# Performance work log

Hardware: AMD Instinct MI355X
Metric: run time of the kernel (lower is better)

## Reference

```python
import jax, jax.numpy as jnp
import numpy as np

_N = 512
_L = 65536


def setup_inputs() -> dict:
    key = jax.random.key(0)
    ks = jax.random.split(key, 11)
    N, L = _N, _L
    sc = 1.0 / np.sqrt(N)  # lecun-normal style scaling
    f = lambda k, s: jax.random.normal(k, s, dtype=jnp.float32)
    return {
        # stable DPLR spectrum: negative real parts
        "Lambda_re": -(jax.random.uniform(ks[0], (N,), dtype=jnp.float32) + 0.1),
        "Lambda_im": f(ks[1], (N,)),
        "p_re": f(ks[2], (N,)), "p_im": f(ks[3], (N,)),
        "q_re": f(ks[4], (N,)), "q_im": f(ks[5], (N,)),
        "Vc_re": f(ks[6], (N, N)) * sc, "Vc_im": f(ks[7], (N, N)) * sc,
        "Ct": f(ks[8], (1, N, 2)) * sc,
        "B": f(ks[9], (N, 1)) * sc,
        "log_step": jax.random.uniform(ks[10], (1,), dtype=jnp.float32)
                    * (np.log(0.1) - np.log(0.001)) + np.log(0.001),
        "L": L,
    }


def reference(Lambda_re, Lambda_im, p_re, p_im, q_re, q_im,
              Vc_re, Vc_im, Ct, B, log_step, L):
    Lambda = Lambda_re + 1j * Lambda_im            # (N,)
    p = p_re + 1j * p_im                           # (N,)
    q = q_re + 1j * q_im                           # (N,)
    Vc = Vc_re + 1j * Vc_im                        # (N,N)
    Ct_c = Ct[..., 0] + 1j * Ct[..., 1]            # (1,N)
    Bc = (Vc @ B.astype(Vc.dtype)).ravel()         # (N,) complex, B = Vc @ B
    step = jnp.exp(log_step)[0]

    # aterm = (Ct*, q*), bterm = (B, p)
    a0 = Ct_c.conj().ravel()
    a1 = q.conj()
    b0 = Bc
    b1 = p

    # roots of unity
    Omega = jnp.exp(-2j * jnp.pi * (jnp.arange(L) / L))   # (L,)
    g = (2.0 / step) * ((1.0 - Omega) / (1.0 + Omega))    # (L,) bilinear transform
    c = 2.0 / (1.0 + Omega)                               # (L,)

    # single fused Cauchy pass: resolvent (L,N) contracted with all 4 rank-1 terms
    r = 1.0 / (g[:, None] - Lambda[None, :])               # (L,N)
    terms = jnp.stack([a0 * b0, a0 * b1, a1 * b0, a1 * b1], axis=1)  # (N,4)
    K = r @ terms                                          # (L,4): k00,k01,k10,k11
    k00, k01, k10, k11 = K[:, 0], K[:, 1], K[:, 2], K[:, 3]

    atRoots = c * (k00 - k01 * (1.0 / (1.0 + k11)) * k10)  # Woodbury correction
    out = jnp.fft.ifft(atRoots, L).reshape(L)
    return out.real
```

## Files before the change

### kernel.cpp

```cpp
#include <hip/hip_runtime.h>
#include <math.h>

constexpr int WS_TERMS = 0;
constexpr int WS_ZT    = 8192;

__device__ __forceinline__ float sin2pi(float x) { return __builtin_amdgcn_sinf(x); }
__device__ __forceinline__ float cos2pi(float x) { return __builtin_amdgcn_cosf(x); }

__global__ __launch_bounds__(256) void k_setup(
    const float* __restrict__ Lr, const float* __restrict__ Li,
    const float* __restrict__ pr, const float* __restrict__ pi,
    const float* __restrict__ qr, const float* __restrict__ qi,
    const float* __restrict__ Vr, const float* __restrict__ Vi,
    const float* __restrict__ Ct, const float* __restrict__ Bv,
    const float* __restrict__ log_step,
    float* __restrict__ terms)
{
    __shared__ float red[8];
    int n = blockIdx.x;
    int t = threadIdx.x;
    float b0 = Bv[t], b1 = Bv[t + 256];
    float sr = fmaf(Vr[n*512 + t], b0, Vr[n*512 + t + 256] * b1);
    float si = fmaf(Vi[n*512 + t], b0, Vi[n*512 + t + 256] * b1);
    #pragma unroll
    for (int off = 32; off > 0; off >>= 1) {
        sr += __shfl_down(sr, off, 64);
        si += __shfl_down(si, off, 64);
    }
    if ((t & 63) == 0) { red[(t >> 6)*2] = sr; red[(t >> 6)*2 + 1] = si; }
    __syncthreads();
    if (t == 0) {
        float b0r = red[0] + red[2] + red[4] + red[6];
        float b0i = red[1] + red[3] + red[5] + red[7];
        double step = exp((double)log_step[0]);
        float t2s = (float)(2.0 / step);
        float lr  = Lr[n];
        float a0r = Ct[2*n], a0i = -Ct[2*n+1];
        float a1r = qr[n],   a1i = -qi[n];
        float b1r = pr[n],   b1i = pi[n];
        float* tm = terms + n * 12;
        tm[0]  = -lr;                 tm[1]  = Li[n];
        tm[2]  = a0r*b0r - a0i*b0i;   tm[3]  = a0r*b0i + a0i*b0r;
        tm[4]  = a0r*b1r - a0i*b1i;   tm[5]  = a0r*b1i + a0i*b1r;
        tm[6]  = a1r*b0r - a1i*b0i;   tm[7]  = a1r*b0i + a1i*b0r;
        tm[8]  = a1r*b1r - a1i*b1i;   tm[9]  = a1r*b1i + a1i*b1r;
        tm[10] = lr*lr;               tm[11] = t2s;
    }
}

__global__ __launch_bounds__(512, 8) void k_mainA(
    const float* __restrict__ terms,
    float* __restrict__ ZTf)
{
    __shared__ float buf[6144];
    int tid = threadIdx.x;
    int b   = blockIdx.x;
    int l1      = b >> 2;
    int quarter = b & 3;

    {
        float4* dst = (float4*)buf;
        const float4* src = (const float4*)terms;
        #pragma unroll
        for (int i = 0; i < 3; ++i) dst[tid + 512*i] = src[tid + 512*i];
    }

    int u     = tid & 63;
    int chunk = tid >> 6;
    int l2    = quarter*64 + u;
    int l     = l1 + 256*l2;

    float tv2 = (float)l * (1.0f / 131072.0f);
    float sn  = sin2pi(tv2), cn = cos2pi(tv2);
    float T   = sn / cn;
    __syncthreads();
    float t2s = buf[11];
    float g_i = t2s * T;
    if (!(fabsf(T) <= 1.0e6f)) { g_i = 3e30f; T = 0.f; }

    float ac[8];
    #pragma unroll
    for (int c = 0; c < 8; ++c) ac[c] = 0.f;

    const float4* t4 = (const float4*)buf + chunk * 64 * 3;
    #pragma unroll 4
    for (int n = 0; n < 64; ++n) {
        float4 Aq = t4[n*3 + 0];
        float4 Bq = t4[n*3 + 1];
        float4 Cq = t4[n*3 + 2];
        float di = g_i - Aq.y;
        float dd = fmaf(di, di, Cq.z);
        float iv = __builtin_amdgcn_rcpf(dd);
        float rr = Aq.x * iv;
        float ri = -di * iv;
        ac[0] = fmaf(rr, Aq.z, ac[0]); ac[0] = fmaf(-ri, Aq.w, ac[0]);
        ac[1] = fmaf(rr, Aq.w, ac[1]); ac[1] = fmaf( ri, Aq.z, ac[1]);
        ac[2] = fmaf(rr, Bq.x, ac[2]); ac[2] = fmaf(-ri, Bq.y, ac[2]);
        ac[3] = fmaf(rr, Bq.y, ac[3]); ac[3] = fmaf( ri, Bq.x, ac[3]);
        ac[4] = fmaf(rr, Bq.z, ac[4]); ac[4] = fmaf(-ri, Bq.w, ac[4]);
        ac[5] = fmaf(rr, Bq.w, ac[5]); ac[5] = fmaf( ri, Bq.z, ac[5]);
        ac[6] = fmaf(rr, Cq.x, ac[6]); ac[6] = fmaf(-ri, Cq.y, ac[6]);
        ac[7] = fmaf(rr, Cq.y, ac[7]); ac[7] = fmaf( ri, Cq.x, ac[7]);
    }
    __syncthreads();

    if (chunk >= 4) {
        float* p = buf + (chunk - 4) * 576 + u * 9;
        #pragma unroll
        for (int c = 0; c < 8; ++c) p[c] = ac[c];
    }
    __syncthreads();
    if (chunk < 4) {
        float* p = buf + chunk * 576 + u * 9;
        #pragma unroll
        for (int c = 0; c < 8; ++c) p[c] += ac[c];
    }
    __syncthreads();

    {
        int a = (tid >> 3) * 9 + (tid & 7);
        buf[2304 + a] = buf[a] + buf[576 + a] + buf[1152 + a] + buf[1728 + a];
    }
    __syncthreads();

    if (tid < 64) {
        const float* rd = buf + 2304 + tid * 9;
        float s0r = rd[0], s0i = rd[1], s1r = rd[2], s1i = rd[3];
        float s2r = rd[4], s2i = rd[5], s3r = rd[6], s3i = rd[7];
        float e1r = 1.f + s3r, e1i = s3i;
        float eiv = 1.0f / fmaf(e1r, e1r, e1i * e1i);
        float m_r = s1r * s2r - s1i * s2i;
        float m_i = s1r * s2i + s1i * s2r;
        float q_r = (m_r * e1r + m_i * e1i) * eiv;
        float q_i = (m_i * e1r - m_r * e1i) * eiv;
        float u_r = s0r - q_r;
        float u_i = s0i - q_i;
        ((float2*)buf)[tid] = make_float2(u_r - T * u_i, u_i + T * u_r);
    }
    __syncthreads();

    {
        int t1 = tid & 255;
        int s  = tid >> 8;
        int j0 = s * 32;
        int mm0 = ((quarter*64 + j0) * t1) & 255;
        float curR = cos2pi((float)mm0 * (1.0f/256.0f));
        float curI = sin2pi((float)mm0 * (1.0f/256.0f));
        float rotR = cos2pi((float)t1 * (1.0f/256.0f));
        float rotI = sin2pi((float)t1 * (1.0f/256.0f));
        const float2* xrow = (const float2*)buf;
        float yr = 0.f, yi = 0.f;
        #pragma unroll 8
        for (int j = j0; j < j0 + 32; ++j) {
            float2 x = xrow[j];
            yr = fmaf(x.x, curR, yr); yr = fmaf(-x.y, curI, yr);
            yi = fmaf(x.x, curI, yi); yi = fmaf( x.y, curR, yi);
            float nR = curR * rotR - curI * rotI;
            float nI = curR * rotI + curI * rotR;
            curR = nR; curI = nI;
        }
        ((float2*)(buf + 128))[tid] = make_float2(yr, yi);
    }
    __syncthreads();
    if (tid < 256) {
        const float2* pA = (const float2*)(buf + 128);
        float2 p0 = pA[tid], p1 = pA[tid + 256];
        float Yr = p0.x + p1.x;
        float Yi = p0.y + p1.y;
        int mm = (l1 * tid) & 65535;
        float tv = (float)mm * (1.0f / 65536.0f);
        float twR = cos2pi(tv), twI = sin2pi(tv);
        ((float2*)(ZTf + quarter * 131072))[tid * 256 + l1] =
            make_float2(Yr * twR - Yi * twI, Yr * twI + Yi * twR);
    }
}

__global__ __launch_bounds__(256) void k_fftB(
    const float* __restrict__ ZTf, float* __restrict__ out)
{
    __shared__ float buf2[768];
    int tid = threadIdx.x;
    int b   = blockIdx.x;
    int t1 = b >> 2;
    int qT = b & 3;
    {
        float2 z = make_float2(0.f, 0.f);
        #pragma unroll
        for (int q = 0; q < 4; ++q) {
            float2 v = ((const float2*)(ZTf + q * 131072))[t1 * 256 + tid];
            z.x += v.x; z.y += v.y;
        }
        ((float2*)buf2)[tid] = z;
    }
    int k2 = tid & 63;
    int s  = tid >> 6;
    int t2 = qT * 64 + k2;
    int m0 = (s * t2) & 3;
    float curR = (m0 == 0) ? 1.f : (m0 == 2 ? -1.f : 0.f);
    float curI = (m0 == 1) ? 1.f : (m0 == 3 ? -1.f : 0.f);
    float rotR = cos2pi((float)t2 * (1.0f / 256.0f));
    float rotI = sin2pi((float)t2 * (1.0f / 256.0f));
    __syncthreads();
    const float2* zrow = (const float2*)buf2;
    float o = 0.f;
    #pragma unroll 8
    for (int j = s * 64; j < s * 64 + 64; ++j) {
        float2 z = zrow[j];
        o = fmaf(z.x, curR, o);
        o = fmaf(-z.y, curI, o);
        float nR = curR * rotR - curI * rotI;
        float nI = curR * rotI + curI * rotR;
        curR = nR; curI = nI;
    }
    buf2[512 + tid] = o;
    __syncthreads();
    if (tid < 64) {
        float sum = buf2[512+tid] + buf2[512+tid+64] + buf2[512+tid+128] + buf2[512+tid+192];
        out[t1 + 256 * (qT * 64 + tid)] = sum * (1.0f / 65536.0f);
    }
}

extern "C" void kernel_launch(void* const* d_in, const int* in_sizes, int n_in,
                              void* d_out, int out_size, void* d_ws, size_t ws_size,
                              hipStream_t stream)
{
    const float* Lambda_re = (const float*)d_in[0];
    const float* Lambda_im = (const float*)d_in[1];
    const float* p_re      = (const float*)d_in[2];
    const float* p_im      = (const float*)d_in[3];
    const float* q_re      = (const float*)d_in[4];
    const float* q_im      = (const float*)d_in[5];
    const float* Vc_re     = (const float*)d_in[6];
    const float* Vc_im     = (const float*)d_in[7];
    const float* Ct        = (const float*)d_in[8];
    const float* Bv        = (const float*)d_in[9];
    const float* log_step  = (const float*)d_in[10];

    float* wsf   = (float*)d_ws;
    float* terms = wsf + WS_TERMS;
    float* ZT    = wsf + WS_ZT;
    float* outp  = (float*)d_out;

    k_setup<<<512, 256, 0, stream>>>(Lambda_re, Lambda_im, p_re, p_im, q_re, q_im,
                                     Vc_re, Vc_im, Ct, Bv, log_step, terms);
    k_mainA<<<1024, 512, 0, stream>>>(terms, ZT);
    k_fftB<<<1024, 256, 0, stream>>>(ZT, outp);
}
```

Measured before the change: 106.6 us.

## Interleave term pairs in shared memory to enable packed float2 FMA math

The per-pole term table is laid out as pairs of poles, with matching fields interleaved (even/odd), and the main Cauchy loop processes two poles per iteration. Two accumulator sets are kept as float2 so the compiler can emit packed FP32 instructions (v_pk_fma_f32) on CDNA, roughly halving the VALU issue count for the reduction. This costs twice the accumulator registers and a final horizontal add, and relies on the compiler actually packing the operations.

```diff
diff --git a/kernel.cpp b/kernel.cpp
--- a/kernel.cpp
+++ b/kernel.cpp
@@ -38,13 +38,15 @@
         float a0r = Ct[2*n], a0i = -Ct[2*n+1];
         float a1r = qr[n],   a1i = -qi[n];
         float b1r = pr[n],   b1i = pi[n];
-        float* tm = terms + n * 12;
-        tm[0]  = -lr;                 tm[1]  = Li[n];
-        tm[2]  = a0r*b0r - a0i*b0i;   tm[3]  = a0r*b0i + a0i*b0r;
-        tm[4]  = a0r*b1r - a0i*b1i;   tm[5]  = a0r*b1i + a0i*b1r;
-        tm[6]  = a1r*b0r - a1i*b0i;   tm[7]  = a1r*b0i + a1i*b0r;
-        tm[8]  = a1r*b1r - a1i*b1i;   tm[9]  = a1r*b1i + a1i*b1r;
-        tm[10] = lr*lr;               tm[11] = t2s;
+        float* tm = terms + (n >> 1) * 24;
+        int par = n & 1;
+        tm[0  + par] = -lr;               tm[2  + par] = Li[n];
+        tm[4  + par] = a0r*b0r - a0i*b0i; tm[6  + par] = a0r*b0i + a0i*b0r;
+        tm[8  + par] = a0r*b1r - a0i*b1i; tm[10 + par] = a0r*b1i + a0i*b1r;
+        tm[12 + par] = a1r*b0r - a1i*b0i; tm[14 + par] = a1r*b0i + a1i*b0r;
+        tm[16 + par] = a1r*b1r - a1i*b1i; tm[18 + par] = a1r*b1i + a1i*b1r;
+        tm[20 + par] = lr*lr;
+        if (par == 0) { tm[22] = t2s; tm[23] = 0.f; }
     }
 }
 
@@ -74,34 +76,47 @@
     float sn  = sin2pi(tv2), cn = cos2pi(tv2);
     float T   = sn / cn;
     __syncthreads();
-    float t2s = buf[11];
+    float t2s = buf[22];
     float g_i = t2s * T;
     if (!(fabsf(T) <= 1.0e6f)) { g_i = 3e30f; T = 0.f; }
 
-    float ac[8];
-    #pragma unroll
-    for (int c = 0; c < 8; ++c) ac[c] = 0.f;
-
-    const float4* t4 = (const float4*)buf + chunk * 64 * 3;
+    float2 a0 = {0.f,0.f}, a1 = {0.f,0.f}, a2 = {0.f,0.f}, a3 = {0.f,0.f};
+    float2 a4 = {0.f,0.f}, a5 = {0.f,0.f}, a6 = {0.f,0.f}, a7 = {0.f,0.f};
+
+    const float4* t4 = (const float4*)buf + chunk * 32 * 6;
     #pragma unroll 4
-    for (int n = 0; n < 64; ++n) {
-        float4 Aq = t4[n*3 + 0];
-        float4 Bq = t4[n*3 + 1];
-        float4 Cq = t4[n*3 + 2];
-        float di = g_i - Aq.y;
-        float dd = fmaf(di, di, Cq.z);
-        float iv = __builtin_amdgcn_rcpf(dd);
-        float rr = Aq.x * iv;
-        float ri = -di * iv;
-        ac[0] = fmaf(rr, Aq.z, ac[0]); ac[0] = fmaf(-ri, Aq.w, ac[0]);
-        ac[1] = fmaf(rr, Aq.w, ac[1]); ac[1] = fmaf( ri, Aq.z, ac[1]);
-        ac[2] = fmaf(rr, Bq.x, ac[2]); ac[2] = fmaf(-ri, Bq.y, ac[2]);
-        ac[3] = fmaf(rr, Bq.y, ac[3]); ac[3] = fmaf( ri, Bq.x, ac[3]);
-        ac[4] = fmaf(rr, Bq.z, ac[4]); ac[4] = fmaf(-ri, Bq.w, ac[4]);
-        ac[5] = fmaf(rr, Bq.w, ac[5]); ac[5] = fmaf( ri, Bq.z, ac[5]);
-        ac[6] = fmaf(rr, Cq.x, ac[6]); ac[6] = fmaf(-ri, Cq.y, ac[6]);
-        ac[7] = fmaf(rr, Cq.y, ac[7]); ac[7] = fmaf( ri, Cq.x, ac[7]);
-    }
+    for (int p = 0; p < 32; ++p) {
+        float4 q0 = t4[p*6 + 0];
+        float4 q1 = t4[p*6 + 1];
+        float4 q2 = t4[p*6 + 2];
+        float4 q3 = t4[p*6 + 3];
+        float4 q4 = t4[p*6 + 4];
+        float4 q5 = t4[p*6 + 5];
+        float2 di, dd, iv, rr, ri;
+        di.x = g_i - q0.z;                  di.y = g_i - q0.w;
+        dd.x = fmaf(di.x, di.x, q5.x);      dd.y = fmaf(di.y, di.y, q5.y);
+        iv.x = __builtin_amdgcn_rcpf(dd.x); iv.y = __builtin_amdgcn_rcpf(dd.y);
+        rr.x = q0.x * iv.x;                 rr.y = q0.y * iv.y;
+        ri.x = -di.x * iv.x;                ri.y = -di.y * iv.y;
+        a0.x = fmaf(rr.x, q1.x, a0.x);  a0.y = fmaf(rr.y, q1.y, a0.y);
+        a0.x = fmaf(-ri.x, q1.z, a0.x); a0.y = fmaf(-ri.y, q1.w, a0.y);
+        a1.x = fmaf(rr.x, q1.z, a1.x);  a1.y = fmaf(rr.y, q1.w, a1.y);
+        a1.x = fmaf( ri.x, q1.x, a1.x); a1.y = fmaf( ri.y, q1.y, a1.y);
+        a2.x = fmaf(rr.x, q2.x, a2.x);  a2.y = fmaf(rr.y, q2.y, a2.y);
+        a2.x = fmaf(-ri.x, q2.z, a2.x); a2.y = fmaf(-ri.y, q2.w, a2.y);
+        a3.x = fmaf(rr.x, q2.z, a3.x);  a3.y = fmaf(rr.y, q2.w, a3.y);
+        a3.x = fmaf( ri.x, q2.x, a3.x); a3.y = fmaf( ri.y, q2.y, a3.y);
+        a4.x = fmaf(rr.x, q3.x, a4.x);  a4.y = fmaf(rr.y, q3.y, a4.y);
+        a4.x = fmaf(-ri.x, q3.z, a4.x); a4.y = fmaf(-ri.y, q3.w, a4.y);
+        a5.x = fmaf(rr.x, q3.z, a5.x);  a5.y = fmaf(rr.y, q3.w, a5.y);
+        a5.x = fmaf( ri.x, q3.x, a5.x); a5.y = fmaf( ri.y, q3.y, a5.y);
+        a6.x = fmaf(rr.x, q4.x, a6.x);  a6.y = fmaf(rr.y, q4.y, a6.y);
+        a6.x = fmaf(-ri.x, q4.z, a6.x); a6.y = fmaf(-ri.y, q4.w, a6.y);
+        a7.x = fmaf(rr.x, q4.z, a7.x);  a7.y = fmaf(rr.y, q4.w, a7.y);
+        a7.x = fmaf( ri.x, q4.x, a7.x); a7.y = fmaf( ri.y, q4.y, a7.y);
+    }
+    float ac[8] = { a0.x + a0.y, a1.x + a1.y, a2.x + a2.y, a3.x + a3.y,
+                    a4.x + a4.y, a5.x + a5.y, a6.x + a6.y, a7.x + a7.y };
     __syncthreads();
 
     if (chunk >= 4) {
```

Result: slower. 116.2 us (+8.9%).
